# Optimization experiments

Hardware: AMD Instinct MI355X
Metric: run time of the kernel (lower is better)

Reference implementation:

```python
import jax, jax.numpy as jnp
import numpy as np

K = 3
HEADS = 6
EMBED = 192
KD = EMBED // HEADS  # 32
SCALE = float(KD) ** -0.5


def setup_inputs() -> dict:
    key = jax.random.key(0)
    ks = jax.random.split(key, 5)
    B, H, W, C = 8, 252, 192, 64
    x = jax.random.normal(ks[0], (B, H, W, C), dtype=jnp.float32)
    v_w = jax.random.normal(ks[1], (C, EMBED), dtype=jnp.float32) * (C ** -0.5)
    attn_w = jax.random.normal(ks[2], (C, K ** 4 * HEADS), dtype=jnp.float32) * (C ** -0.5)
    attn_b = jnp.zeros((K ** 4 * HEADS,), dtype=jnp.float32)
    out_w = jax.random.normal(ks[3], (EMBED, EMBED), dtype=jnp.float32) * (EMBED ** -0.5)
    out_b = jnp.zeros((EMBED,), dtype=jnp.float32)
    return {"x": x, "v_w": v_w, "attn_w": attn_w, "attn_b": attn_b,
            "out_w": out_w, "out_b": out_b}


def reference(x, v_w, attn_w, attn_b, out_w, out_b):
    B, H, W, C = x.shape
    hh, ww = -(-H // K), -(-W // K)          # ceil division
    ph, pw = hh * K - H, ww * K - W          # bottom/right zero padding
    xp = jnp.pad(x, ((0, 0), (0, ph), (0, pw), (0, 0))) if (ph or pw) else x

    # value branch: unfold into k*k windows -> [B, hh, ww, heads, k^2, kd]
    v = xp @ v_w
    v = v.reshape(B, hh, K, ww, K, HEADS, KD)
    v = v.transpose(0, 1, 3, 5, 2, 4, 6).reshape(B, hh, ww, HEADS, K * K, KD)

    # attention branch: k x k average pool (stride k) then dense to k^4*heads
    pooled = xp.reshape(B, hh, K, ww, K, C).mean(axis=(2, 4))  # [B, hh, ww, C]
    attn = (pooled @ attn_w + attn_b) * SCALE
    attn = attn.reshape(B, hh, ww, HEADS, K * K, K * K)
    attn = jax.nn.softmax(attn, axis=-1)

    # windowed attention: [.., k^2, k^2] @ [.., k^2, kd]
    out = attn @ v                                             # [B, hh, ww, heads, k^2, kd]

    # fold back to spatial layout, drop padding
    out = out.reshape(B, hh, ww, HEADS, K, K, KD)
    out = out.transpose(0, 1, 4, 2, 5, 3, 6).reshape(B, hh * K, ww * K, EMBED)
    out = out[:, :H, :W, :]
    return out @ out_w + out_b
```

## Files before the change

### kernel.cpp

```cpp
#include <hip/hip_runtime.h>
#include <hip/hip_bf16.h>

#define NB   8
#define NH   252
#define NW   192
#define NC   64
#define HHD  84
#define WWD  64
#define NE   192
#define NO   486
#define NWIN (NB*HHD*WWD)
#define SCALE_F 0.17677669529663687f

typedef __bf16 bf16x8 __attribute__((ext_vector_type(8)));
typedef float floatx4 __attribute__((ext_vector_type(4)));

__device__ __attribute__((aligned(16))) __hip_bfloat16 g_WT[NE * 384];
__device__ __attribute__((aligned(16))) __hip_bfloat16 g_awT[NO * 64];

__device__ __forceinline__ bf16x8 bf16x8_zero() {
    bf16x8 z;
    #pragma unroll
    for (int j = 0; j < 8; ++j) z[j] = (__bf16)0.f;
    return z;
}

__global__ __launch_bounds__(256) void kt_prep(
    const float* __restrict__ vw, const float* __restrict__ ow,
    const float* __restrict__ aw)
{
    int t = blockIdx.x * 256 + threadIdx.x;
    if (t < NE * 384) {
        int e  = t / 384;
        int hc = t - e * 384;
        int h  = hc >> 6;
        int c  = hc & 63;
        float s = 0.f;
        #pragma unroll
        for (int d = 0; d < 32; ++d)
            s = fmaf(vw[c * NE + h * 32 + d], ow[(h * 32 + d) * NE + e], s);
        g_WT[e * 384 + hc] = __float2bfloat16(s);
    } else {
        int tt = t - NE * 384;
        if (tt < NO * 64) {
            int n = tt >> 6;
            int c = tt & 63;
            g_awT[tt] = __float2bfloat16(aw[c * NO + n]);
        }
    }
}

__global__ __launch_bounds__(256, 3) void ka_fused(
    const float* __restrict__ x,
    const float* __restrict__ attn_b,
    const float* __restrict__ out_b,
    float* __restrict__ out)
{
    __shared__ __attribute__((aligned(16))) __bf16 xwT[64 * 104];
    __shared__ __attribute__((aligned(16))) __bf16 pooledB[8 * 64];
    __shared__ __attribute__((aligned(16))) __bf16 attnS[8 * 486];
    __shared__ __attribute__((aligned(16))) __bf16 attnBD[80 * 104];
    __shared__ __attribute__((aligned(16))) __bf16 Ph[80 * 72];

    const int tid  = threadIdx.x;
    const int lane = tid & 63;
    const int wv   = tid >> 6;
    const int m16  = lane & 15;
    const int quad = lane >> 4;
    const int wbase = blockIdx.x * 8;

    const int bB   = wbase / 5376;
    const int remB = wbase - bB * 5376;
    const int iB   = remB >> 6;
    const int jB   = remB & 63;
    const int xbase = ((bB * NH + iB * 3) * NW + jB * 3) * NC;

    #pragma unroll
    for (int it = 0; it < 18; ++it) {
        int row = it * 4 + wv;
        int win = row / 9;
        int q   = row - win * 9;
        int pr  = q / 3;
        int pc  = q - pr * 3;
        float xv = x[xbase + (pr * NW + win * 3 + pc) * NC + lane];
        xwT[lane * 104 + row] = (__bf16)xv;
    }
    {
        int rr = tid >> 2, ss = tid & 3;
        *(uint4*)(&xwT[rr * 104 + 72 + ss * 8]) = make_uint4(0u, 0u, 0u, 0u);
    }
    #pragma unroll
    for (int it = 0; it < 5; ++it) {
        int ch = it * 256 + tid;
        if (ch < 1040) *(uint4*)(&attnBD[ch * 8]) = make_uint4(0u, 0u, 0u, 0u);
    }
    __syncthreads();

    #pragma unroll
    for (int it = 0; it < 2; ++it) {
        int win = it * 4 + wv;
        float s = 0.f;
        #pragma unroll
        for (int q = 0; q < 9; ++q) s += (float)xwT[lane * 104 + win * 9 + q];
        pooledB[win * 64 + lane] = (__bf16)(s * (1.f / 9.f));
    }
    __syncthreads();

    {
        bf16x8 afragP[2];
        #pragma unroll
        for (int ks = 0; ks < 2; ++ks)
            afragP[ks] = *(const bf16x8*)(&pooledB[m16 * 64 + ks * 32 + quad * 8]);
        const __bf16* Aw = (const __bf16*)g_awT;
        #pragma unroll
        for (int i = 0; i < 8; ++i) {
            int tile = wv * 8 + i;
            int n = tile * 16 + m16;
            bool nvalid = (tile < 31) && (n < NO);
            bf16x8 b0 = nvalid ? *(const bf16x8*)(Aw + n * 64 + quad * 8)      : bf16x8_zero();
            bf16x8 b1 = nvalid ? *(const bf16x8*)(Aw + n * 64 + 32 + quad * 8) : bf16x8_zero();
            floatx4 acc;
            acc[0] = 0.f; acc[1] = 0.f; acc[2] = 0.f; acc[3] = 0.f;
            acc = __builtin_amdgcn_mfma_f32_16x16x32_bf16(afragP[0], b0, acc, 0, 0, 0);
            acc = __builtin_amdgcn_mfma_f32_16x16x32_bf16(afragP[1], b1, acc, 0, 0, 0);
            if (nvalid && quad < 2) {
                float bn = attn_b[n];
                #pragma unroll
                for (int r = 0; r < 4; ++r)
                    attnS[(quad * 4 + r) * NO + n] = (__bf16)((acc[r] + bn) * SCALE_F);
            }
        }
    }
    __syncthreads();

    #pragma unroll
    for (int it = 0; it < 2; ++it) {
        int t = it * 256 + tid;
        if (t < 432) {
            int win = t / 54;
            int g = t - win * 54;
            __bf16* a = &attnS[win * NO + g * 9];
            float v[9];
            v[0] = (float)a[0];
            float m = v[0];
            #pragma unroll
            for (int q = 1; q < 9; ++q) { v[q] = (float)a[q]; m = fmaxf(m, v[q]); }
            float s = 0.f;
            #pragma unroll
            for (int q = 0; q < 9; ++q) { v[q] = __expf(v[q] - m); s += v[q]; }
            float inv = 1.f / s;
            #pragma unroll
            for (int q = 0; q < 9; ++q) a[q] = (__bf16)(v[q] * inv);
        }
    }
    __syncthreads();

    bf16x8 bfragX[3];
    #pragma unroll
    for (int ks = 0; ks < 3; ++ks)
        bfragX[ks] = *(const bf16x8*)(&xwT[(wv * 16 + m16) * 104 + ks * 32 + quad * 8]);

    float bias[3];
    #pragma unroll
    for (int nt = 0; nt < 3; ++nt) bias[nt] = out_b[wv * 48 + nt * 16 + m16];

    floatx4 accF[5][3];
    #pragma unroll
    for (int mt = 0; mt < 5; ++mt)
        #pragma unroll
        for (int nt = 0; nt < 3; ++nt) {
            accF[mt][nt][0] = 0.f; accF[mt][nt][1] = 0.f;
            accF[mt][nt][2] = 0.f; accF[mt][nt][3] = 0.f;
        }

    const __bf16* Wt = (const __bf16*)g_WT;

    for (int h = 0; h < 6; ++h) {
        #pragma unroll
        for (int it = 0; it < 3; ++it) {
            int t = it * 256 + tid;
            if (t < 648) {
                int win = t / 81;
                int r81 = t - win * 81;
                int p = r81 / 9;
                int q = r81 - p * 9;
                attnBD[(win * 9 + p) * 104 + win * 9 + q] = attnS[win * NO + h * 81 + r81];
            }
        }
        __syncthreads();

        {
            floatx4 accP[5];
            #pragma unroll
            for (int mt = 0; mt < 5; ++mt) {
                accP[mt][0] = 0.f; accP[mt][1] = 0.f; accP[mt][2] = 0.f; accP[mt][3] = 0.f;
            }
            #pragma unroll
            for (int ks = 0; ks < 3; ++ks)
                #pragma unroll
                for (int mt = 0; mt < 5; ++mt) {
                    bf16x8 af = *(const bf16x8*)(&attnBD[(mt * 16 + m16) * 104 + ks * 32 + quad * 8]);
                    accP[mt] = __builtin_amdgcn_mfma_f32_16x16x32_bf16(af, bfragX[ks], accP[mt], 0, 0, 0);
                }
            #pragma unroll
            for (int mt = 0; mt < 5; ++mt)
                #pragma unroll
                for (int r = 0; r < 4; ++r)
                    Ph[(mt * 16 + quad * 4 + r) * 72 + wv * 16 + m16] = (__bf16)accP[mt][r];
        }
        __syncthreads();

        #pragma unroll
        for (int ks = 0; ks < 2; ++ks) {
            bf16x8 bw[3];
            #pragma unroll
            for (int nt = 0; nt < 3; ++nt)
                bw[nt] = *(const bf16x8*)(Wt + (wv * 48 + nt * 16 + m16) * 384 + h * 64 + ks * 32 + quad * 8);
            #pragma unroll
            for (int mt = 0; mt < 5; ++mt) {
                bf16x8 af = *(const bf16x8*)(&Ph[(mt * 16 + m16) * 72 + ks * 32 + quad * 8]);
                #pragma unroll
                for (int nt = 0; nt < 3; ++nt)
                    accF[mt][nt] = __builtin_amdgcn_mfma_f32_16x16x32_bf16(af, bw[nt], accF[mt][nt], 0, 0, 0);
            }
        }
    }

    const int obase = ((bB * NH + iB * 3) * NW + jB * 3) * NE;
    #pragma unroll
    for (int mt = 0; mt < 5; ++mt)
        #pragma unroll
        for (int r = 0; r < 4; ++r) {
            int row = mt * 16 + quad * 4 + r;
            if (row < 72) {
                int win = row / 9;
                int p = row - win * 9;
                int pr = p / 3;
                int pc = p - pr * 3;
                int base = obase + (pr * NW + win * 3 + pc) * NE;
                #pragma unroll
                for (int nt = 0; nt < 3; ++nt)
                    out[base + wv * 48 + nt * 16 + m16] = accF[mt][nt][r] + bias[nt];
            }
        }
}

extern "C" void kernel_launch(void* const* d_in, const int* in_sizes, int n_in,
                              void* d_out, int out_size, void* d_ws, size_t ws_size,
                              hipStream_t stream)
{
    const float* x      = (const float*)d_in[0];
    const float* v_w    = (const float*)d_in[1];
    const float* attn_w = (const float*)d_in[2];
    const float* attn_b = (const float*)d_in[3];
    const float* out_w  = (const float*)d_in[4];
    const float* out_b  = (const float*)d_in[5];
    float* out = (float*)d_out;
    (void)d_ws; (void)ws_size; (void)in_sizes; (void)n_in; (void)out_size;

    hipLaunchKernelGGL(kt_prep, dim3(410), dim3(256), 0, stream, v_w, out_w, attn_w);
    hipLaunchKernelGGL(ka_fused, dim3(NWIN / 8), dim3(256), 0, stream,
                       x, attn_b, out_b, out);
}
```

Baseline: 494.6 us.

## Replace block-diagonal attention matmul with banded per-tile attention layout

Pads each window's 9 positions to 10 so that every 16-row tile of the block-diagonal attention matrix touches only a 32-wide band of columns. The softmaxed attention is written straight into per-head, per-tile compact A fragments. This cuts the attention-times-value step from 15 to 5 MFMAs per head and removes the per-head scatter into a zeroed block-diagonal buffer along with one barrier per head. In exchange it adds index arithmetic, more zero padding, and reuses the Ph buffer for the pooled values.

```diff
diff --git a/kernel.cpp b/kernel.cpp
--- a/kernel.cpp
+++ b/kernel.cpp
@@ -13,6 +13,7 @@
 #define SCALE_F 0.17677669529663687f
 
 typedef __bf16 bf16x8 __attribute__((ext_vector_type(8)));
+typedef __bf16 bf16x4 __attribute__((ext_vector_type(4)));
 typedef float floatx4 __attribute__((ext_vector_type(4)));
 
 __device__ __attribute__((aligned(16))) __hip_bfloat16 g_WT[NE * 384];
@@ -23,6 +24,12 @@
     #pragma unroll
     for (int j = 0; j < 8; ++j) z[j] = (__bf16)0.f;
     return z;
+}
+
+__device__ __forceinline__ int koff(int t) {
+    int v = 16 * t - 8;
+    v = v < 0 ? 0 : v;
+    return v > 48 ? 48 : v;
 }
 
 __global__ __launch_bounds__(256) void kt_prep(
@@ -56,11 +63,11 @@
     const float* __restrict__ out_b,
     float* __restrict__ out)
 {
-    __shared__ __attribute__((aligned(16))) __bf16 xwT[64 * 104];
-    __shared__ __attribute__((aligned(16))) __bf16 pooledB[8 * 64];
-    __shared__ __attribute__((aligned(16))) __bf16 attnS[8 * 486];
-    __shared__ __attribute__((aligned(16))) __bf16 attnBD[80 * 104];
+    __shared__ __attribute__((aligned(16))) __bf16 xwT[64 * 88];
+    __shared__ __attribute__((aligned(16))) __bf16 attnA[6 * 5 * 16 * 32];
     __shared__ __attribute__((aligned(16))) __bf16 Ph[80 * 72];
+
+    __bf16* pooledB = Ph;
 
     const int tid  = threadIdx.x;
     const int lane = tid & 63;
@@ -76,32 +83,37 @@
     const int xbase = ((bB * NH + iB * 3) * NW + jB * 3) * NC;
 
     #pragma unroll
-    for (int it = 0; it < 18; ++it) {
-        int row = it * 4 + wv;
-        int win = row / 9;
-        int q   = row - win * 9;
-        int pr  = q / 3;
-        int pc  = q - pr * 3;
-        float xv = x[xbase + (pr * NW + win * 3 + pc) * NC + lane];
-        xwT[lane * 104 + row] = (__bf16)xv;
-    }
-    {
-        int rr = tid >> 2, ss = tid & 3;
-        *(uint4*)(&xwT[rr * 104 + 72 + ss * 8]) = make_uint4(0u, 0u, 0u, 0u);
-    }
-    #pragma unroll
-    for (int it = 0; it < 5; ++it) {
-        int ch = it * 256 + tid;
-        if (ch < 1040) *(uint4*)(&attnBD[ch * 8]) = make_uint4(0u, 0u, 0u, 0u);
-    }
-    __syncthreads();
-
-    #pragma unroll
-    for (int it = 0; it < 2; ++it) {
-        int win = it * 4 + wv;
+    for (int i = 0; i < 5; ++i) {
+        int b4 = i * 4 + wv;
+        bf16x4 pk;
+        #pragma unroll
+        for (int s = 0; s < 4; ++s) {
+            int p10 = b4 * 4 + s;
+            int w = p10 / 10;
+            int q = p10 - w * 10;
+            float xv = 0.f;
+            if (q < 9) {
+                int pr = q / 3;
+                int pc = q - pr * 3;
+                xv = x[xbase + (pr * NW + w * 3 + pc) * NC + lane];
+            }
+            pk[s] = (__bf16)xv;
+        }
+        *(bf16x4*)(&xwT[lane * 88 + b4 * 4]) = pk;
+    }
+    #pragma unroll
+    for (int i = 0; i < 8; ++i) {
+        int ch = i * 256 + tid;
+        if (ch < 1920) *(uint4*)(&attnA[ch * 8]) = make_uint4(0u, 0u, 0u, 0u);
+    }
+    __syncthreads();
+
+    #pragma unroll
+    for (int i = 0; i < 2; ++i) {
+        int win = i * 4 + wv;
         float s = 0.f;
         #pragma unroll
-        for (int q = 0; q < 9; ++q) s += (float)xwT[lane * 104 + win * 9 + q];
+        for (int q = 0; q < 9; ++q) s += (float)xwT[lane * 88 + win * 10 + q];
         pooledB[win * 64 + lane] = (__bf16)(s * (1.f / 9.f));
     }
     __syncthreads();
@@ -125,9 +137,20 @@
             acc = __builtin_amdgcn_mfma_f32_16x16x32_bf16(afragP[1], b1, acc, 0, 0, 0);
             if (nvalid && quad < 2) {
                 float bn = attn_b[n];
-                #pragma unroll
-                for (int r = 0; r < 4; ++r)
-                    attnS[(quad * 4 + r) * NO + n] = (__bf16)((acc[r] + bn) * SCALE_F);
+                int h   = n / 81;
+                int r81 = n - h * 81;
+                int p   = r81 / 9;
+                int q   = r81 - p * 9;
+                #pragma unroll
+                for (int r = 0; r < 4; ++r) {
+                    int win = quad * 4 + r;
+                    int R   = win * 10 + p;
+                    int t   = R >> 4;
+                    int rl  = R & 15;
+                    int col = win * 10 + q - koff(t);
+                    attnA[((h * 5 + t) * 16 + rl) * 32 + col] =
+                        (__bf16)((acc[r] + bn) * SCALE_F);
+                }
             }
         }
     }
@@ -135,30 +158,35 @@
 
     #pragma unroll
     for (int it = 0; it < 2; ++it) {
-        int t = it * 256 + tid;
-        if (t < 432) {
-            int win = t / 54;
-            int g = t - win * 54;
-            __bf16* a = &attnS[win * NO + g * 9];
+        int g = it * 256 + tid;
+        if (g < 432) {
+            int win  = g / 54;
+            int rest = g - win * 54;
+            int h = rest / 9;
+            int p = rest - h * 9;
+            int R  = win * 10 + p;
+            int t  = R >> 4;
+            int rl = R & 15;
+            int cb = win * 10 - koff(t);
+            __bf16* a = &attnA[((h * 5 + t) * 16 + rl) * 32 + cb];
             float v[9];
-            v[0] = (float)a[0];
-            float m = v[0];
-            #pragma unroll
-            for (int q = 1; q < 9; ++q) { v[q] = (float)a[q]; m = fmaxf(m, v[q]); }
-            float s = 0.f;
-            #pragma unroll
-            for (int q = 0; q < 9; ++q) { v[q] = __expf(v[q] - m); s += v[q]; }
-            float inv = 1.f / s;
+            float m = -1e30f;
+            #pragma unroll
+            for (int q = 0; q < 9; ++q) { v[q] = (float)a[q]; m = fmaxf(m, v[q]); }
+            float ssum = 0.f;
+            #pragma unroll
+            for (int q = 0; q < 9; ++q) { v[q] = __expf(v[q] - m); ssum += v[q]; }
+            float inv = 1.f / ssum;
             #pragma unroll
             for (int q = 0; q < 9; ++q) a[q] = (__bf16)(v[q] * inv);
         }
     }
     __syncthreads();
 
-    bf16x8 bfragX[3];
-    #pragma unroll
-    for (int ks = 0; ks < 3; ++ks)
-        bfragX[ks] = *(const bf16x8*)(&xwT[(wv * 16 + m16) * 104 + ks * 32 + quad * 8]);
+    bf16x8 bfragX[5];
+    #pragma unroll
+    for (int t = 0; t < 5; ++t)
+        bfragX[t] = *(const bf16x8*)(&xwT[(wv * 16 + m16) * 88 + koff(t) + quad * 8]);
 
     float bias[3];
     #pragma unroll
@@ -175,33 +203,17 @@
 
     const __bf16* Wt = (const __bf16*)g_WT;
 
+    #pragma unroll
     for (int h = 0; h < 6; ++h) {
-        #pragma unroll
-        for (int it = 0; it < 3; ++it) {
-            int t = it * 256 + tid;
-            if (t < 648) {
-                int win = t / 81;
-                int r81 = t - win * 81;
-                int p = r81 / 9;
-                int q = r81 - p * 9;
-                attnBD[(win * 9 + p) * 104 + win * 9 + q] = attnS[win * NO + h * 81 + r81];
-            }
-        }
-        __syncthreads();
-
         {
             floatx4 accP[5];
             #pragma unroll
             for (int mt = 0; mt < 5; ++mt) {
-                accP[mt][0] = 0.f; accP[mt][1] = 0.f; accP[mt][2] = 0.f; accP[mt][3] = 0.f;
-            }
-            #pragma unroll
-            for (int ks = 0; ks < 3; ++ks)
-                #pragma unroll
-                for (int mt = 0; mt < 5; ++mt) {
-                    bf16x8 af = *(const bf16x8*)(&attnBD[(mt * 16 + m16) * 104 + ks * 32 + quad * 8]);
-                    accP[mt] = __builtin_amdgcn_mfma_f32_16x16x32_bf16(af, bfragX[ks], accP[mt], 0, 0, 0);
-                }
+                accP[mt][0] = 0.f; accP[mt][1] = 0.f;
+                accP[mt][2] = 0.f; accP[mt][3] = 0.f;
+                bf16x8 af = *(const bf16x8*)(&attnA[((h * 5 + mt) * 16 + m16) * 32 + quad * 8]);
+                accP[mt] = __builtin_amdgcn_mfma_f32_16x16x32_bf16(af, bfragX[mt], accP[mt], 0, 0, 0);
+            }
             #pragma unroll
             for (int mt = 0; mt < 5; ++mt)
                 #pragma unroll
@@ -224,6 +236,7 @@
                     accF[mt][nt] = __builtin_amdgcn_mfma_f32_16x16x32_bf16(af, bw[nt], accF[mt][nt], 0, 0, 0);
             }
         }
+        if (h < 5) __syncthreads();
     }
 
     const int obase = ((bB * NH + iB * 3) * NW + jB * 3) * NE;
@@ -232,9 +245,9 @@
         #pragma unroll
         for (int r = 0; r < 4; ++r) {
             int row = mt * 16 + quad * 4 + r;
-            if (row < 72) {
-                int win = row / 9;
-                int p = row - win * 9;
+            int win = row / 10;
+            int p   = row - win * 10;
+            if (p < 9) {
                 int pr = p / 3;
                 int pc = p - pr * 3;
                 int base = obase + (pr * NW + win * 3 + pc) * NE;
```

New measurement: 558.6 us. 13.0% more time.
